# Kernel optimization log

Hardware: AMD Instinct MI355X
Metric: run time of the kernel (lower is better)

The kernel has to match this reference:

```python
import jax, jax.numpy as jnp
import numpy as np
from functools import partial

# Thresholds from _SamAutomaticMaskGenerator defaults
MASK_THRESHOLD = 0.0
PRED_IOU_THRESH = 0.88
STABILITY_THRESH = 0.95
STABILITY_OFFSET = 1.0
BOX_NMS_THRESH = 0.7

N_MASKS, H, W = 1024, 256, 256  # 32x32 point grid -> 1024 masks; SAM low-res mask size


def setup_inputs() -> dict:
    key = jax.random.key(0)
    k1, k2, k3, k4, k5 = jax.random.split(key, 5)
    # Structured blob logits so stability scores / boxes / NMS behave realistically.
    cy = jax.random.uniform(k1, (N_MASKS,)) * H
    cx = jax.random.uniform(k2, (N_MASKS,)) * W
    r = 20.0 + jax.random.uniform(k3, (N_MASKS,)) * 60.0
    yy = jnp.arange(H, dtype=jnp.float32)[:, None]
    xx = jnp.arange(W, dtype=jnp.float32)[None, :]
    dist = jnp.sqrt((yy - cy[:, None, None]) ** 2 + (xx - cx[:, None, None]) ** 2)  # [N,H,W]
    noise = jax.random.normal(k4, (N_MASKS, H, W), dtype=jnp.float32) * 0.1
    mask_logits = (2.0 * (r[:, None, None] - dist) + noise).astype(jnp.float32)
    iou_preds = jax.random.uniform(k5, (N_MASKS,), dtype=jnp.float32)
    return {"mask_logits": mask_logits, "iou_preds": iou_preds}


def _masks_to_boxes(binary):
    # binary: [N,H,W] bool -> inclusive xyxy boxes [N,4] float32 (empty masks -> zeros),
    # matching SAM's batched_mask_to_box.
    n, h, w = binary.shape
    row_any = binary.any(axis=2)  # [N,H]
    col_any = binary.any(axis=1)  # [N,W]
    ys = jnp.arange(h)
    xs = jnp.arange(w)
    top = jnp.min(jnp.where(row_any, ys, h), axis=1)
    bottom = jnp.max(jnp.where(row_any, ys, -1), axis=1)
    left = jnp.min(jnp.where(col_any, xs, w), axis=1)
    right = jnp.max(jnp.where(col_any, xs, -1), axis=1)
    boxes = jnp.stack([left, top, right, bottom], axis=-1).astype(jnp.float32)
    empty = ~row_any.any(axis=1)
    return jnp.where(empty[:, None], 0.0, boxes)


def _box_iou_one_vs_all(box, boxes):
    # box: [4], boxes: [N,4] xyxy -> iou [N]
    x0 = jnp.maximum(box[0], boxes[:, 0])
    y0 = jnp.maximum(box[1], boxes[:, 1])
    x1 = jnp.minimum(box[2], boxes[:, 2])
    y1 = jnp.minimum(box[3], boxes[:, 3])
    inter = jnp.clip(x1 - x0, 0.0) * jnp.clip(y1 - y0, 0.0)
    area_a = jnp.clip(box[2] - box[0], 0.0) * jnp.clip(box[3] - box[1], 0.0)
    area_b = jnp.clip(boxes[:, 2] - boxes[:, 0], 0.0) * jnp.clip(boxes[:, 3] - boxes[:, 1], 0.0)
    return inter / jnp.maximum(area_a + area_b - inter, 1e-6)


def _greedy_nms(boxes, scores, valid, thresh):
    # Greedy NMS over fixed N, returning a keep mask in original order.
    n = boxes.shape[0]
    order = jnp.argsort(-jnp.where(valid, scores, -jnp.inf))
    b = boxes[order]
    keep0 = valid[order]
    idx = jnp.arange(n)

    def body(i, keep):
        iou = _box_iou_one_vs_all(b[i], b)
        suppress = (iou > thresh) & (idx > i) & keep[i]
        return keep & ~suppress

    keep_sorted = jax.lax.fori_loop(0, n, body, keep0)
    return jnp.zeros((n,), dtype=bool).at[order].set(keep_sorted)


def reference(mask_logits, iou_preds):
    # Stability score: area at (thr+offset) / area at (thr-offset), as in SAM.
    hi = (mask_logits > (MASK_THRESHOLD + STABILITY_OFFSET)).sum(axis=(1, 2)).astype(jnp.float32)
    lo = (mask_logits > (MASK_THRESHOLD - STABILITY_OFFSET)).sum(axis=(1, 2)).astype(jnp.float32)
    stability = hi / jnp.maximum(lo, 1.0)

    binary = mask_logits > MASK_THRESHOLD  # [N,H,W] bool
    valid = (iou_preds > PRED_IOU_THRESH) & (stability >= STABILITY_THRESH)

    boxes = _masks_to_boxes(binary)  # [N,4]
    keep = _greedy_nms(boxes, iou_preds, valid, BOX_NMS_THRESH)  # [N] bool

    # Differentiable summary output: soft masks gated by kept score.
    gated = iou_preds * keep.astype(mask_logits.dtype)  # [N]
    out = jax.nn.sigmoid(mask_logits) * gated[:, None, None]  # [N,H,W]
    return out, keep, boxes
```

## Files before the change

kernel.cpp:

```cpp
#include <hip/hip_runtime.h>
#include <math.h>

#define NMASK 1024
#define HH 256
#define WW 256
#define HW 65536
#define OUT_ELEMS 67108864

__global__ __launch_bounds__(256) void stats_kernel(
    const float* __restrict__ logits, int* __restrict__ stats) {
  const int m = blockIdx.x;
  const int t = threadIdx.x;
  const float4* __restrict__ p = (const float4*)(logits + (size_t)m * HW);

  int hi = 0, lo = 0;
  int miny = HH, maxy = -1, minx = WW, maxx = -1;

  for (int k = 0; k < 64; ++k) {
    const int f = k * 256 + t;
    const float4 v = p[f];
    const int y = f >> 6;
    const int x0 = (f & 63) << 2;

    const bool p0 = v.x > 0.0f, p1 = v.y > 0.0f, p2 = v.z > 0.0f, p3 = v.w > 0.0f;
    hi += (v.x > 1.0f) + (v.y > 1.0f) + (v.z > 1.0f) + (v.w > 1.0f);
    lo += (v.x > -1.0f) + (v.y > -1.0f) + (v.z > -1.0f) + (v.w > -1.0f);
    if (p0 | p1 | p2 | p3) {
      miny = min(miny, y);
      maxy = max(maxy, y);
      if (p0) { minx = min(minx, x0);     maxx = max(maxx, x0); }
      if (p1) { minx = min(minx, x0 + 1); maxx = max(maxx, x0 + 1); }
      if (p2) { minx = min(minx, x0 + 2); maxx = max(maxx, x0 + 2); }
      if (p3) { minx = min(minx, x0 + 3); maxx = max(maxx, x0 + 3); }
    }
  }

  for (int off = 32; off; off >>= 1) {
    hi += __shfl_down(hi, off);
    lo += __shfl_down(lo, off);
    miny = min(miny, __shfl_down(miny, off));
    maxy = max(maxy, __shfl_down(maxy, off));
    minx = min(minx, __shfl_down(minx, off));
    maxx = max(maxx, __shfl_down(maxx, off));
  }

  __shared__ int red[4][6];
  const int wv = t >> 6, ln = t & 63;
  if (ln == 0) {
    red[wv][0] = hi;  red[wv][1] = lo;
    red[wv][2] = miny; red[wv][3] = maxy;
    red[wv][4] = minx; red[wv][5] = maxx;
  }
  __syncthreads();
  if (t == 0) {
    int H2 = 0, L2 = 0, mny = HH, mxy = -1, mnx = WW, mxx = -1;
    for (int w = 0; w < 4; ++w) {
      H2 += red[w][0]; L2 += red[w][1];
      mny = min(mny, red[w][2]); mxy = max(mxy, red[w][3]);
      mnx = min(mnx, red[w][4]); mxx = max(mxx, red[w][5]);
    }
    int* s = stats + m * 8;
    s[0] = H2; s[1] = L2; s[2] = mny; s[3] = mxy; s[4] = mnx; s[5] = mxx;
  }
}

__global__ __launch_bounds__(256) void scorerank_kernel(
    const float* __restrict__ iou_preds, const int* __restrict__ stats,
    float* __restrict__ sbox, int* __restrict__ sidx, int* __restrict__ svalid,
    float* __restrict__ boxes_out) {
  __shared__ float ssc[NMASK];
  const int b = blockIdx.x;
  const int t = threadIdx.x;

  for (int j = t; j < NMASK; j += 256) {
    const int* s = stats + j * 8;
    const float stab = (float)s[0] / fmaxf((float)s[1], 1.0f);
    const float iv = iou_preds[j];
    const bool valid = (iv > 0.88f) && (stab >= 0.95f);
    ssc[j] = valid ? iv : -INFINITY;
  }
  __syncthreads();

  const float si = ssc[b];
  int r = 0;
  for (int j = t; j < NMASK; j += 256) {
    const float sj = ssc[j];
    r += (sj > si) || (sj == si && j < b);
  }
  for (int off = 32; off; off >>= 1) r += __shfl_down(r, off);
  __shared__ int red[4];
  if ((t & 63) == 0) red[t >> 6] = r;
  __syncthreads();
  if (t == 0) {
    const int rank = red[0] + red[1] + red[2] + red[3];
    const int* s = stats + b * 8;
    float bx0, by0, bx1, by1;
    if (s[3] < 0) { bx0 = by0 = bx1 = by1 = 0.0f; }
    else { bx0 = (float)s[4]; by0 = (float)s[2]; bx1 = (float)s[5]; by1 = (float)s[3]; }
    sidx[rank] = b;
    svalid[rank] = (si != -INFINITY) ? 1 : 0;
    sbox[rank * 4 + 0] = bx0; sbox[rank * 4 + 1] = by0;
    sbox[rank * 4 + 2] = bx1; sbox[rank * 4 + 3] = by1;
    boxes_out[b * 4 + 0] = bx0; boxes_out[b * 4 + 1] = by0;
    boxes_out[b * 4 + 2] = bx1; boxes_out[b * 4 + 3] = by1;
  }
}

__global__ __launch_bounds__(1024) void iou_kernel(
    const float* __restrict__ sbox, const int* __restrict__ svalid,
    unsigned long long* __restrict__ rows) {
  const int i = blockIdx.x;
  if (!svalid[i]) return;
  const int j = threadIdx.x;
  const float ax0 = sbox[i * 4 + 0], ay0 = sbox[i * 4 + 1];
  const float ax1 = sbox[i * 4 + 2], ay1 = sbox[i * 4 + 3];
  const float bx0 = sbox[j * 4 + 0], by0 = sbox[j * 4 + 1];
  const float bx1 = sbox[j * 4 + 2], by1 = sbox[j * 4 + 3];
  const float x0 = fmaxf(ax0, bx0), y0 = fmaxf(ay0, by0);
  const float x1 = fminf(ax1, bx1), y1 = fminf(ay1, by1);
  const float inter = fmaxf(x1 - x0, 0.0f) * fmaxf(y1 - y0, 0.0f);
  const float aa = fmaxf(ax1 - ax0, 0.0f) * fmaxf(ay1 - ay0, 0.0f);
  const float ab = fmaxf(bx1 - bx0, 0.0f) * fmaxf(by1 - by0, 0.0f);
  const float iou = inter / fmaxf(aa + ab - inter, 1e-6f);
  const bool supp = (iou > 0.7f) && (j > i);
  const unsigned long long b = __ballot(supp);
  if ((j & 63) == 0) rows[i * 16 + (j >> 6)] = b;
}

#define PREF_ROWS 256
__global__ __launch_bounds__(256) void nms_kernel(
    const unsigned long long* __restrict__ rows,
    const int* __restrict__ sidx, const int* __restrict__ svalid,
    const float* __restrict__ iou_preds, float* __restrict__ gated,
    float* __restrict__ keep_out) {
  __shared__ unsigned long long srows[PREF_ROWS * 16];
  const int t = threadIdx.x;
  for (int k = t; k < PREF_ROWS * 16; k += 256) srows[k] = rows[k];
  __syncthreads();
  if (t >= 64) return;
  const int lane = t;

  unsigned long long keepword = 0ull;
  int nv = 0;
  for (int c = 0; c < 16; ++c) {
    const int v = svalid[c * 64 + lane];
    const unsigned long long b = __ballot(v != 0);
    if (lane == c) keepword = b;
    nv += (int)__popcll(b) ? 0 : 0;
    nv += (int)__popcll(b);
  }
  nv >>= 0;

  for (int i = 0; i < nv; ++i) {
    const int w = i >> 6, bit = i & 63;
    const unsigned long long kw = __shfl(keepword, w, 64);
    if ((kw >> bit) & 1ull) {
      if (lane < 16) {
        const unsigned long long r =
            (i < PREF_ROWS) ? srows[i * 16 + lane] : rows[i * 16 + lane];
        keepword &= ~r;
      }
    }
  }

  for (int c = 0; c < 16; ++c) {
    const unsigned long long kw = __shfl(keepword, c, 64);
    const int j = c * 64 + lane;
    const int orig = sidx[j];
    const float kept = ((kw >> lane) & 1ull) ? 1.0f : 0.0f;
    keep_out[orig] = kept;
    gated[orig] = kept * iou_preds[orig];
  }
}

__global__ __launch_bounds__(256) void out_kernel(
    const float* __restrict__ logits, const float* __restrict__ gated,
    float* __restrict__ out) {
  const int b = blockIdx.x;
  const int m = b >> 2;
  const float g = gated[m];
  const size_t base4 = (size_t)m * 16384 + (size_t)(b & 3) * 4096;
  const float4* __restrict__ in4 = (const float4*)logits + base4;
  float4* __restrict__ o4 = (float4*)out + base4;
  const int t = threadIdx.x;
  if (g == 0.0f) {
    const float4 z = {0.0f, 0.0f, 0.0f, 0.0f};
#pragma unroll
    for (int k = 0; k < 16; ++k) o4[t + k * 256] = z;
  } else {
#pragma unroll
    for (int k = 0; k < 16; ++k) {
      const float4 v = in4[t + k * 256];
      float4 r;
      r.x = g / (1.0f + __expf(-v.x));
      r.y = g / (1.0f + __expf(-v.y));
      r.z = g / (1.0f + __expf(-v.z));
      r.w = g / (1.0f + __expf(-v.w));
      o4[t + k * 256] = r;
    }
  }
}

extern "C" void kernel_launch(void* const* d_in, const int* in_sizes, int n_in,
                              void* d_out, int out_size, void* d_ws, size_t ws_size,
                              hipStream_t stream) {
  const float* logits = (const float*)d_in[0];
  const float* iou    = (const float*)d_in[1];

  float* out       = (float*)d_out;
  float* keep_out  = out + OUT_ELEMS;
  float* boxes_out = keep_out + NMASK;

  char* w = (char*)d_ws;
  int*   stats  = (int*)(w);
  float* sbox   = (float*)(w + 32768);
  int*   sidx   = (int*)(w + 49152);
  int*   svalid = (int*)(w + 53248);
  float* gated  = (float*)(w + 57344);
  unsigned long long* rows = (unsigned long long*)(w + 61440);

  stats_kernel<<<NMASK, 256, 0, stream>>>(logits, stats);
  scorerank_kernel<<<NMASK, 256, 0, stream>>>(iou, stats, sbox, sidx, svalid, boxes_out);
  iou_kernel<<<NMASK, 1024, 0, stream>>>(sbox, svalid, rows);
  nms_kernel<<<1, 256, 0, stream>>>(rows, sidx, svalid, iou, gated, keep_out);
  out_kernel<<<NMASK * 4, 256, 0, stream>>>(logits, gated, out);
}
```

Measured before the change: 480.3 us.

## Fuse IoU matrix and NMS into one block; split stats and output grids finer

Merges the IoU-suppression-bitmask kernel and the serial NMS kernel into a single 1024-thread block. It computes rows for the first 512 sorted candidates into shared memory and computes the rare later rows on demand, which removes one launch and the global round trip of the bitmask. The stats kernel now splits each mask across two blocks and writes partial stats that scorerank merges, and the output kernel uses twice as many smaller blocks. Both changes aim for better occupancy on the memory-bound passes. The cost is that the IoU matrix is now computed by a single block instead of across the whole device.

```diff
diff --git a/kernel.cpp b/kernel.cpp
--- a/kernel.cpp
+++ b/kernel.cpp
@@ -6,20 +6,24 @@
 #define WW 256
 #define HW 65536
 #define OUT_ELEMS 67108864
+#define ROWS_CAP 512
 
 __global__ __launch_bounds__(256) void stats_kernel(
-    const float* __restrict__ logits, int* __restrict__ stats) {
-  const int m = blockIdx.x;
-  const int t = threadIdx.x;
-  const float4* __restrict__ p = (const float4*)(logits + (size_t)m * HW);
+    const float* __restrict__ logits, int* __restrict__ pstats) {
+  const int m = blockIdx.x >> 1;
+  const int h = blockIdx.x & 1;
+  const int t = threadIdx.x;
+  const float4* __restrict__ p =
+      (const float4*)(logits + (size_t)m * HW + (size_t)h * (HW / 2));
 
   int hi = 0, lo = 0;
   int miny = HH, maxy = -1, minx = WW, maxx = -1;
 
-  for (int k = 0; k < 64; ++k) {
+#pragma unroll 4
+  for (int k = 0; k < 32; ++k) {
     const int f = k * 256 + t;
     const float4 v = p[f];
-    const int y = f >> 6;
+    const int y = (f >> 6) + h * 128;
     const int x0 = (f & 63) << 2;
 
     const bool p0 = v.x > 0.0f, p1 = v.y > 0.0f, p2 = v.z > 0.0f, p3 = v.w > 0.0f;
@@ -59,13 +63,13 @@
       mny = min(mny, red[w][2]); mxy = max(mxy, red[w][3]);
       mnx = min(mnx, red[w][4]); mxx = max(mxx, red[w][5]);
     }
-    int* s = stats + m * 8;
+    int* s = pstats + blockIdx.x * 8;
     s[0] = H2; s[1] = L2; s[2] = mny; s[3] = mxy; s[4] = mnx; s[5] = mxx;
   }
 }
 
 __global__ __launch_bounds__(256) void scorerank_kernel(
-    const float* __restrict__ iou_preds, const int* __restrict__ stats,
+    const float* __restrict__ iou_preds, const int* __restrict__ pstats,
     float* __restrict__ sbox, int* __restrict__ sidx, int* __restrict__ svalid,
     float* __restrict__ boxes_out) {
   __shared__ float ssc[NMASK];
@@ -73,8 +77,11 @@
   const int t = threadIdx.x;
 
   for (int j = t; j < NMASK; j += 256) {
-    const int* s = stats + j * 8;
-    const float stab = (float)s[0] / fmaxf((float)s[1], 1.0f);
+    const int* a = pstats + (2 * j) * 8;
+    const int* c = pstats + (2 * j + 1) * 8;
+    const int hi = a[0] + c[0];
+    const int lo = a[1] + c[1];
+    const float stab = (float)hi / fmaxf((float)lo, 1.0f);
     const float iv = iou_preds[j];
     const bool valid = (iv > 0.88f) && (stab >= 0.95f);
     ssc[j] = valid ? iv : -INFINITY;
@@ -93,10 +100,13 @@
   __syncthreads();
   if (t == 0) {
     const int rank = red[0] + red[1] + red[2] + red[3];
-    const int* s = stats + b * 8;
+    const int* a = pstats + (2 * b) * 8;
+    const int* c = pstats + (2 * b + 1) * 8;
+    const int mny = min(a[2], c[2]), mxy = max(a[3], c[3]);
+    const int mnx = min(a[4], c[4]), mxx = max(a[5], c[5]);
     float bx0, by0, bx1, by1;
-    if (s[3] < 0) { bx0 = by0 = bx1 = by1 = 0.0f; }
-    else { bx0 = (float)s[4]; by0 = (float)s[2]; bx1 = (float)s[5]; by1 = (float)s[3]; }
+    if (mxy < 0) { bx0 = by0 = bx1 = by1 = 0.0f; }
+    else { bx0 = (float)mnx; by0 = (float)mny; bx1 = (float)mxx; by1 = (float)mxy; }
     sidx[rank] = b;
     svalid[rank] = (si != -INFINITY) ? 1 : 0;
     sbox[rank * 4 + 0] = bx0; sbox[rank * 4 + 1] = by0;
@@ -106,90 +116,100 @@
   }
 }
 
-__global__ __launch_bounds__(1024) void iou_kernel(
-    const float* __restrict__ sbox, const int* __restrict__ svalid,
-    unsigned long long* __restrict__ rows) {
-  const int i = blockIdx.x;
-  if (!svalid[i]) return;
-  const int j = threadIdx.x;
-  const float ax0 = sbox[i * 4 + 0], ay0 = sbox[i * 4 + 1];
-  const float ax1 = sbox[i * 4 + 2], ay1 = sbox[i * 4 + 3];
-  const float bx0 = sbox[j * 4 + 0], by0 = sbox[j * 4 + 1];
-  const float bx1 = sbox[j * 4 + 2], by1 = sbox[j * 4 + 3];
+__device__ __forceinline__ bool supp_bit(const float* bx, int i, int j) {
+  const float ax0 = bx[i * 4 + 0], ay0 = bx[i * 4 + 1];
+  const float ax1 = bx[i * 4 + 2], ay1 = bx[i * 4 + 3];
+  const float bx0 = bx[j * 4 + 0], by0 = bx[j * 4 + 1];
+  const float bx1 = bx[j * 4 + 2], by1 = bx[j * 4 + 3];
   const float x0 = fmaxf(ax0, bx0), y0 = fmaxf(ay0, by0);
   const float x1 = fminf(ax1, bx1), y1 = fminf(ay1, by1);
   const float inter = fmaxf(x1 - x0, 0.0f) * fmaxf(y1 - y0, 0.0f);
   const float aa = fmaxf(ax1 - ax0, 0.0f) * fmaxf(ay1 - ay0, 0.0f);
   const float ab = fmaxf(bx1 - bx0, 0.0f) * fmaxf(by1 - by0, 0.0f);
   const float iou = inter / fmaxf(aa + ab - inter, 1e-6f);
-  const bool supp = (iou > 0.7f) && (j > i);
-  const unsigned long long b = __ballot(supp);
-  if ((j & 63) == 0) rows[i * 16 + (j >> 6)] = b;
-}
-
-#define PREF_ROWS 256
-__global__ __launch_bounds__(256) void nms_kernel(
-    const unsigned long long* __restrict__ rows,
-    const int* __restrict__ sidx, const int* __restrict__ svalid,
-    const float* __restrict__ iou_preds, float* __restrict__ gated,
-    float* __restrict__ keep_out) {
-  __shared__ unsigned long long srows[PREF_ROWS * 16];
-  const int t = threadIdx.x;
-  for (int k = t; k < PREF_ROWS * 16; k += 256) srows[k] = rows[k];
-  __syncthreads();
-  if (t >= 64) return;
-  const int lane = t;
-
-  unsigned long long keepword = 0ull;
-  int nv = 0;
-  for (int c = 0; c < 16; ++c) {
-    const int v = svalid[c * 64 + lane];
-    const unsigned long long b = __ballot(v != 0);
-    if (lane == c) keepword = b;
-    nv += (int)__popcll(b) ? 0 : 0;
-    nv += (int)__popcll(b);
-  }
-  nv >>= 0;
-
-  for (int i = 0; i < nv; ++i) {
-    const int w = i >> 6, bit = i & 63;
-    const unsigned long long kw = __shfl(keepword, w, 64);
-    if ((kw >> bit) & 1ull) {
-      if (lane < 16) {
-        const unsigned long long r =
-            (i < PREF_ROWS) ? srows[i * 16 + lane] : rows[i * 16 + lane];
-        keepword &= ~r;
+  return (iou > 0.7f) && (j > i);
+}
+
+__global__ __launch_bounds__(1024) void iounms_kernel(
+    const float* __restrict__ sboxg, const int* __restrict__ sidxg,
+    const int* __restrict__ svalidg, const float* __restrict__ iou_preds,
+    float* __restrict__ gated, float* __restrict__ keep_out) {
+  __shared__ float bx[NMASK * 4];
+  __shared__ int sv[NMASK];
+  __shared__ int si[NMASK];
+  __shared__ unsigned long long rows[ROWS_CAP * 16];
+  __shared__ unsigned long long keepw[16];
+
+  const int t = threadIdx.x;
+  const int wave = t >> 6, lane = t & 63;
+
+  for (int k = t; k < NMASK * 4; k += 1024) bx[k] = sboxg[k];
+  for (int k = t; k < NMASK; k += 1024) { sv[k] = svalidg[k]; si[k] = sidxg[k]; }
+  __syncthreads();
+
+  for (int i = wave; i < ROWS_CAP; i += 16) {
+    if (!sv[i]) continue;
+    for (int c = 0; c < 16; ++c) {
+      const int j = c * 64 + lane;
+      const unsigned long long b = __ballot(supp_bit(bx, i, j));
+      if (lane == 0) rows[i * 16 + c] = b;
+    }
+  }
+  __syncthreads();
+
+  if (wave == 0) {
+    unsigned long long keepword = 0ull;
+    int nv = 0;
+    for (int c = 0; c < 16; ++c) {
+      const unsigned long long b = __ballot(sv[c * 64 + lane] != 0);
+      if (lane == c) keepword = b;
+      nv += (int)__popcll(b);
+    }
+    for (int i = 0; i < nv; ++i) {
+      const int w = i >> 6, bit = i & 63;
+      const unsigned long long kw = __shfl(keepword, w, 64);
+      if ((kw >> bit) & 1ull) {
+        if (i < ROWS_CAP) {
+          if (lane < 16) keepword &= ~rows[i * 16 + lane];
+        } else {
+          unsigned long long myrow = 0ull;
+          for (int c = 0; c < 16; ++c) {
+            const int j = c * 64 + lane;
+            const unsigned long long b = __ballot(supp_bit(bx, i, j));
+            if (lane == c) myrow = b;
+          }
+          if (lane < 16) keepword &= ~myrow;
+        }
       }
     }
-  }
-
-  for (int c = 0; c < 16; ++c) {
-    const unsigned long long kw = __shfl(keepword, c, 64);
-    const int j = c * 64 + lane;
-    const int orig = sidx[j];
-    const float kept = ((kw >> lane) & 1ull) ? 1.0f : 0.0f;
-    keep_out[orig] = kept;
-    gated[orig] = kept * iou_preds[orig];
-  }
+    if (lane < 16) keepw[lane] = keepword;
+  }
+  __syncthreads();
+
+  const unsigned long long kw = keepw[t >> 6];
+  const float kept = ((kw >> (t & 63)) & 1ull) ? 1.0f : 0.0f;
+  const int orig = si[t];
+  keep_out[orig] = kept;
+  gated[orig] = kept * iou_preds[orig];
 }
 
 __global__ __launch_bounds__(256) void out_kernel(
     const float* __restrict__ logits, const float* __restrict__ gated,
     float* __restrict__ out) {
   const int b = blockIdx.x;
-  const int m = b >> 2;
+  const int m = b >> 3;
   const float g = gated[m];
-  const size_t base4 = (size_t)m * 16384 + (size_t)(b & 3) * 4096;
+  const size_t base4 = (size_t)m * 16384 + (size_t)(b & 7) * 2048;
   const float4* __restrict__ in4 = (const float4*)logits + base4;
   float4* __restrict__ o4 = (float4*)out + base4;
   const int t = threadIdx.x;
   if (g == 0.0f) {
     const float4 z = {0.0f, 0.0f, 0.0f, 0.0f};
 #pragma unroll
-    for (int k = 0; k < 16; ++k) o4[t + k * 256] = z;
+    for (int k = 0; k < 8; ++k) o4[t + k * 256] = z;
   } else {
 #pragma unroll
-    for (int k = 0; k < 16; ++k) {
+    for (int k = 0; k < 8; ++k) {
       const float4 v = in4[t + k * 256];
       float4 r;
       r.x = g / (1.0f + __expf(-v.x));
@@ -212,16 +232,14 @@
   float* boxes_out = keep_out + NMASK;
 
   char* w = (char*)d_ws;
-  int*   stats  = (int*)(w);
-  float* sbox   = (float*)(w + 32768);
-  int*   sidx   = (int*)(w + 49152);
-  int*   svalid = (int*)(w + 53248);
-  float* gated  = (float*)(w + 57344);
-  unsigned long long* rows = (unsigned long long*)(w + 61440);
-
-  stats_kernel<<<NMASK, 256, 0, stream>>>(logits, stats);
-  scorerank_kernel<<<NMASK, 256, 0, stream>>>(iou, stats, sbox, sidx, svalid, boxes_out);
-  iou_kernel<<<NMASK, 1024, 0, stream>>>(sbox, svalid, rows);
-  nms_kernel<<<1, 256, 0, stream>>>(rows, sidx, svalid, iou, gated, keep_out);
-  out_kernel<<<NMASK * 4, 256, 0, stream>>>(logits, gated, out);
-}
+  int*   pstats = (int*)(w);
+  float* sbox   = (float*)(w + 65536);
+  int*   sidx   = (int*)(w + 81920);
+  int*   svalid = (int*)(w + 86016);
+  float* gated  = (float*)(w + 90112);
+
+  stats_kernel<<<NMASK * 2, 256, 0, stream>>>(logits, pstats);
+  scorerank_kernel<<<NMASK, 256, 0, stream>>>(iou, pstats, sbox, sidx, svalid, boxes_out);
+  iounms_kernel<<<1, 1024, 0, stream>>>(sbox, sidx, svalid, iou, gated, keep_out);
+  out_kernel<<<NMASK * 8, 256, 0, stream>>>(logits, gated, out);
+}
```

Result: no change. 489.1 us (+1.8%).
